# Optimization experiments

Hardware: AMD Instinct MI355X
Metric: run time of the kernel (lower is better)

## Reference

```python
import jax, jax.numpy as jnp
import numpy as np

C_STD = 64                 # len(standard_1020)
CH_NUMS = (1, 4, 16, 64)   # multi-scale channel counts (ms_ch_lst / ch_nums)
BETA = 0.25
DECAY = 0.99
RESI = 0.5                 # abs(quant_resi) for shared Phi


def l2norm(t, eps=1e-12):
    return t / jnp.maximum(jnp.linalg.norm(t, axis=-1, keepdims=True), eps)


def phi_apply(h_LND, w, b):
    # Phi: y = (1-r)*h + r*Conv1d(h), conv over the channel-position axis, feature dim D
    x = jnp.swapaxes(h_LND, 1, 2)                      # (L, D, Nch)
    y = jax.lax.conv_general_dilated(x, w, (1,), 'SAME',
                                     dimension_numbers=('NCH', 'OIH', 'NCH'))
    y = y + b[None, :, None]
    y = jnp.swapaxes(y, 1, 2)                          # (L, Nch, D)
    return h_LND * (1.0 - RESI) + y * RESI


def setup_inputs() -> dict:
    key = jax.random.key(0)
    ks = jax.random.split(key, 5)
    B, T, D, V = 64, 16, 256, 8192
    N = T * C_STD
    z = jax.random.normal(ks[0], (B, N, D), jnp.float32)
    # per-sample permutation of the 64 standard channel ids in the first C_STD slots
    perm = jnp.argsort(jax.random.uniform(ks[1], (B, C_STD)), axis=1).astype(jnp.int32)
    input_chans = jnp.concatenate([perm, jnp.zeros((B, N - C_STD), jnp.int32)], axis=1)
    # tokens ordered time-major: token j has time index j // C_STD
    input_time = jnp.broadcast_to((jnp.arange(N) // C_STD)[None, :], (B, N)).astype(jnp.int32)
    embedding = jax.random.normal(ks[2], (V, D), jnp.float32) * (D ** -0.5 / 36.0)
    phi_w = jax.random.normal(ks[3], (D, D, 3), jnp.float32) * (1.0 / np.sqrt(3.0 * D))
    phi_b = jnp.zeros((D,), jnp.float32)
    cluster_size = jnp.zeros((V,), jnp.float32)
    return {"z": z, "input_chans": input_chans, "input_time": input_time,
            "embedding": embedding, "phi_w": phi_w, "phi_b": phi_b,
            "cluster_size": cluster_size}


def reference(z, input_chans, input_time, embedding, phi_w, phi_b, cluster_size):
    B, N, D = z.shape
    T = N // C_STD
    V = embedding.shape[0]
    z = l2norm(z)
    chans = input_chans[:, :C_STD]                     # (B, 64) channel ids
    # ch_trans: scatter tokens into standard channel layout -> (L, C_STD, D), L = B*T
    z_btcd = z.reshape(B, T, C_STD, D)
    z_LND = jax.vmap(lambda zb, cb: jnp.zeros((T, C_STD, D), z.dtype).at[:, cb].set(zb))(z_btcd, chans)
    z_LND = z_LND.reshape(B * T, C_STD, D)
    L = B * T

    f_no_grad = jax.lax.stop_gradient(z_LND)
    f_rest = f_no_grad
    f_hat = jnp.zeros_like(f_rest)
    e_n = l2norm(embedding)                            # normalized codebook (V, D)

    SN = len(CH_NUMS)
    loss = jnp.zeros((), z.dtype)
    counts = jnp.zeros((V,), z.dtype)
    idx_list = []
    for g in CH_NUMS:                                  # multi-scale residual VQ over channels
        rest_g = f_rest.reshape(L, g, C_STD // g, D).mean(axis=2)   # group_chans_by_mean
        q = l2norm(rest_g)
        logits = jnp.einsum('lgd,vd->lgv', q, e_n)     # cosine sim == -0.5*l2 dist + const
        idx = jnp.argmax(logits, axis=-1)              # (L, g)
        idx_list.append(idx)
        h_g = e_n[idx]                                 # codebook lookup (L, g, D)
        h = jnp.repeat(h_g, C_STD // g, axis=1)        # expand_chans_by_copy -> (L, 64, D)
        h = phi_apply(h, phi_w, phi_b)                 # shared Phi residual conv
        f_hat = f_hat + h
        f_rest = f_rest - h
        loss = loss + BETA * jnp.mean((jax.lax.stop_gradient(f_hat) - z_LND) ** 2) \
                    + jnp.mean((f_hat - f_no_grad) ** 2)
        counts = counts.at[idx.reshape(-1)].add(1.0)   # EMA cluster-size scatter
    loss = loss / SN

    # straight-through: value = f_hat, gradient flows to z
    f_hat_st = jax.lax.stop_gradient(f_hat) + (z_LND - f_no_grad)
    # ch_intrans: gather back to original per-sample channel ordering
    zq_btcd = jax.vmap(lambda fb, cb: fb[:, cb])(f_hat_st.reshape(B, T, C_STD, D), chans)
    z_q = zq_btcd.reshape(B, N, D)

    cluster_size_new = DECAY * cluster_size + (1.0 - DECAY) * counts
    idx_all = jnp.concatenate(idx_list, axis=1)        # (L, sum(CH_NUMS))
    return z_q, loss, idx_all, cluster_size_new
```

## Files before the change

### kernel.cpp

```cpp
#include <hip/hip_runtime.h>

#define D_DIM 256
#define V_DIM 8192
#define L_DIM 1024
#define NROW 65536
#define NELEM 16777216

#define OUT_LOSS 16777216
#define OUT_IDX  16777217
#define OUT_CS   16864257

#define EN_OFF    ((size_t)0)
#define ENH_OFF   ((size_t)2097152)
#define ESUM_OFF  ((size_t)3145728)
#define E0_OFF    ((size_t)5242880)
#define E2_OFF    ((size_t)7340032)
#define WSUM_OFF  ((size_t)9437184)
#define W0_OFF    ((size_t)9502720)
#define W2_OFF    ((size_t)9568256)
#define FREST_OFF ((size_t)9633792)
#define QF_OFF    ((size_t)26411008)
#define QH_OFF    ((size_t)43188224)
#define PTOP_OFF  ((size_t)51576832)
#define IDXI_OFF  ((size_t)52625408)
#define CNT_OFF   ((size_t)52712448)
#define LOSSP_OFF ((size_t)52720640)
#define RNORM_OFF ((size_t)52722688)
#define INV_OFF   ((size_t)52788224)

typedef __attribute__((ext_vector_type(8))) short bf16x8;
typedef __attribute__((ext_vector_type(4))) float f32x4;

__device__ __forceinline__ unsigned int umaxu(unsigned int a, unsigned int b) { return a > b ? a : b; }
__device__ __forceinline__ unsigned int uminu(unsigned int a, unsigned int b) { return a < b ? a : b; }

__device__ __forceinline__ unsigned short f2b(float x) {
    unsigned int u = __float_as_uint(x);
    unsigned int r = (u + 0x7FFFu + ((u >> 16) & 1u)) >> 16;
    return (unsigned short)r;
}

__device__ __forceinline__ void gl_lds16(const void* g, void* l) {
    __builtin_amdgcn_global_load_lds(
        (const __attribute__((address_space(1))) unsigned int*)g,
        (__attribute__((address_space(3))) unsigned int*)l, 16, 0, 0);
}

__device__ __forceinline__ float blk_reduce_sum(float v, float* sb) {
#pragma unroll
    for (int off = 32; off; off >>= 1) v += __shfl_down(v, off, 64);
    const int w = threadIdx.x >> 6;
    if ((threadIdx.x & 63) == 0) sb[w] = v;
    __syncthreads();
    return sb[0] + sb[1] + sb[2] + sb[3];
}

__global__ void k_norm_embed(const float* __restrict__ emb, float* __restrict__ en,
                             unsigned short* __restrict__ enh) {
    __shared__ float sb[4];
    const int v = blockIdx.x, o = threadIdx.x;
    const float x = emb[(size_t)v * 256 + o];
    const float ss = blk_reduce_sum(x * x, sb);
    const float sc = 1.0f / fmaxf(sqrtf(ss), 1e-12f);
    const float y = x * sc;
    en[(size_t)v * 256 + o] = y;
    enh[(size_t)v * 256 + o] = f2b(y);
}

__global__ void k_prep_w(const float* __restrict__ pw, float* __restrict__ wsum,
                         float* __restrict__ w0, float* __restrict__ w2) {
    const int i = blockIdx.x * 256 + threadIdx.x;
    const float a = pw[(size_t)i * 3 + 0];
    const float b = pw[(size_t)i * 3 + 1];
    const float c = pw[(size_t)i * 3 + 2];
    wsum[i] = a + b + c; w0[i] = a; w2[i] = c;
}

__global__ __launch_bounds__(256) void k_phi_gemm(
    const float* __restrict__ en, const float* __restrict__ wsum,
    const float* __restrict__ w0, const float* __restrict__ w2,
    float* __restrict__ esum, float* __restrict__ e0, float* __restrict__ e2) {
    __shared__ __align__(16) float smem[4096];
    float (*As)[128] = (float (*)[128])smem;
    float (*Bs)[128] = (float (*)[128])(smem + 2048);
    const float* Bm; float* Cm;
    if (blockIdx.z == 0)      { Bm = wsum; Cm = esum; }
    else if (blockIdx.z == 1) { Bm = w0;   Cm = e0;   }
    else                      { Bm = w2;   Cm = e2;   }
    const int tid = threadIdx.x, tx = tid & 15, ty = tid >> 4;
    const int rowbase = blockIdx.x * 128, colbase = blockIdx.y * 128;
    float acc[8][8];
#pragma unroll
    for (int r = 0; r < 8; r++)
#pragma unroll
        for (int c = 0; c < 8; c++) acc[r][c] = 0.f;
    for (int kb = 0; kb < 256; kb += 16) {
        __syncthreads();
        {
            const int lr = tid >> 1, k0 = (tid & 1) << 3;
            const float4* ap = (const float4*)(en + ((size_t)(rowbase + lr)) * 256 + kb + k0);
            const float4 a0 = ap[0], a1 = ap[1];
            const float4* bp = (const float4*)(Bm + ((size_t)(colbase + lr)) * 256 + kb + k0);
            const float4 b0 = bp[0], b1 = bp[1];
            As[k0+0][lr]=a0.x; As[k0+1][lr]=a0.y; As[k0+2][lr]=a0.z; As[k0+3][lr]=a0.w;
            As[k0+4][lr]=a1.x; As[k0+5][lr]=a1.y; As[k0+6][lr]=a1.z; As[k0+7][lr]=a1.w;
            Bs[k0+0][lr]=b0.x; Bs[k0+1][lr]=b0.y; Bs[k0+2][lr]=b0.z; Bs[k0+3][lr]=b0.w;
            Bs[k0+4][lr]=b1.x; Bs[k0+5][lr]=b1.y; Bs[k0+6][lr]=b1.z; Bs[k0+7][lr]=b1.w;
        }
        __syncthreads();
#pragma unroll
        for (int k = 0; k < 16; k++) {
            const float4 av0 = *(const float4*)&As[k][ty << 3];
            const float4 av1 = *(const float4*)&As[k][(ty << 3) + 4];
            const float4 bv0 = *(const float4*)&Bs[k][tx << 3];
            const float4 bv1 = *(const float4*)&Bs[k][(tx << 3) + 4];
            const float a[8] = {av0.x, av0.y, av0.z, av0.w, av1.x, av1.y, av1.z, av1.w};
            const float b[8] = {bv0.x, bv0.y, bv0.z, bv0.w, bv1.x, bv1.y, bv1.z, bv1.w};
#pragma unroll
            for (int r = 0; r < 8; r++)
#pragma unroll
                for (int c = 0; c < 8; c++) acc[r][c] = fmaf(a[r], b[c], acc[r][c]);
        }
    }
#pragma unroll
    for (int r = 0; r < 8; r++) {
        float4 o0 = {acc[r][0], acc[r][1], acc[r][2], acc[r][3]};
        float4 o1 = {acc[r][4], acc[r][5], acc[r][6], acc[r][7]};
        float* cp = Cm + ((size_t)(rowbase + (ty << 3) + r)) * 256 + colbase + (tx << 3);
        *(float4*)cp = o0; *(float4*)(cp + 4) = o1;
    }
}

__global__ void k_invperm(const int* __restrict__ ichans, int* __restrict__ inv) {
    const int b = blockIdx.x, c = threadIdx.x;
    inv[(b << 6) + ichans[(b << 10) + c]] = c;
}

__global__ void k_scatter(const float* __restrict__ z, const int* __restrict__ ichans,
                          float* __restrict__ frest, float* __restrict__ rnorm) {
    __shared__ float sb[4];
    const int zrow = blockIdx.x;
    const int b = zrow >> 10, n = zrow & 1023;
    const int t = n >> 6, c = n & 63;
    const int o = threadIdx.x;
    const float x = z[(size_t)zrow * 256 + o];
    const float ss = blk_reduce_sum(x * x, sb);
    const float sc = 1.0f / fmaxf(sqrtf(ss), 1e-12f);
    const int ch = ichans[(b << 10) + c];
    frest[((size_t)(((b << 4) + t) * 64 + ch)) * 256 + o] = x * sc;
    if (o == 0) rnorm[zrow] = sc;
}

__global__ void k_groupq(const float* __restrict__ frest, float* __restrict__ qf,
                         unsigned short* __restrict__ qh, int g, int s) {
    __shared__ float sb[4];
    const int r = blockIdx.x;
    const int l = r / g, j = r - l * g;
    const int o = threadIdx.x;
    const float* base = frest + ((size_t)l * 64 + (size_t)j * s) * 256 + o;
    float acc = 0.f;
    for (int cc = 0; cc < s; cc++) acc += base[(size_t)cc * 256];
    acc *= (1.0f / (float)s);
    const float ss = blk_reduce_sum(acc * acc, sb);
    const float sc = 1.0f / fmaxf(sqrtf(ss), 1e-12f);
    const float qv = acc * sc;
    qf[(size_t)r * 256 + o] = qv;
    qh[(size_t)r * 256 + o] = f2b(qv);
}

__global__ __launch_bounds__(256, 3) void k_amax1(
    const unsigned short* __restrict__ qh, const unsigned short* __restrict__ enh,
    uint2* __restrict__ ptop, int NC, int colsPerChunk) {
    __shared__ unsigned short As[4096];
    __shared__ unsigned short Bs[4096];
    const int tid = threadIdx.x;
    const int lane = tid & 63;
    const int m = lane & 15, q4 = lane >> 4;
    const int w = tid >> 6;
    const int wr = w >> 1, wc = w & 1;
    const int rowbase = blockIdx.x * 128;
    const int chunk = blockIdx.y;
    const int srow = tid >> 2, sgr = tid & 3;

    const unsigned short* qa0 = qh + (size_t)(rowbase + srow) * 256 + sgr * 8;
    const unsigned short* qa1 = qa0 + 64 * 256;
    unsigned short* lA0 = &As[tid * 8];
    unsigned short* lA1 = &As[2048 + tid * 8];
    unsigned short* lB0 = &Bs[tid * 8];
    unsigned short* lB1 = &Bs[2048 + tid * 8];

    unsigned int t1[4][4], t2[4][4];
#pragma unroll
    for (int i = 0; i < 4; i++)
#pragma unroll
        for (int r = 0; r < 4; r++) { t1[i][r] = 0u; t2[i][r] = 0u; }

    const int ntiles = colsPerChunk >> 7;
    for (int nt = 0; nt < ntiles; nt++) {
        const int colchunk = chunk * colsPerChunk + nt * 128;
        const unsigned short* ba0 = enh + (size_t)(colchunk + srow) * 256 + sgr * 8;
        const unsigned short* ba1 = ba0 + 64 * 256;
        f32x4 acc[4][4];
#pragma unroll
        for (int i = 0; i < 4; i++)
#pragma unroll
            for (int j = 0; j < 4; j++) acc[i][j] = (f32x4){0.f, 0.f, 0.f, 0.f};

        for (int kb = 0; kb < 256; kb += 32) {
            __syncthreads();
            gl_lds16(qa0 + kb, lA0);
            gl_lds16(qa1 + kb, lA1);
            gl_lds16(ba0 + kb, lB0);
            gl_lds16(ba1 + kb, lB1);
            __syncthreads();
            bf16x8 af[4], bfr[4];
#pragma unroll
            for (int i = 0; i < 4; i++)
                af[i] = *(const bf16x8*)&As[(wr * 64 + i * 16 + m) * 32 + q4 * 8];
#pragma unroll
            for (int j = 0; j < 4; j++)
                bfr[j] = *(const bf16x8*)&Bs[(wc * 64 + j * 16 + m) * 32 + q4 * 8];
#pragma unroll
            for (int i = 0; i < 4; i++)
#pragma unroll
                for (int j = 0; j < 4; j++)
                    acc[i][j] = __builtin_amdgcn_mfma_f32_16x16x32_bf16(af[i], bfr[j], acc[i][j], 0, 0, 0);
        }
#pragma unroll
        for (int j = 0; j < 4; j++) {
            const unsigned int ct = 8191u - (unsigned int)(colchunk + wc * 64 + j * 16 + m);
#pragma unroll
            for (int i = 0; i < 4; i++)
#pragma unroll
                for (int r = 0; r < 4; r++) {
                    const float wv = acc[i][j][r] + 1.25f;
                    const unsigned int cand = (__float_as_uint(wv) & 0xFFFFE000u) | ct;
                    const unsigned int nb1 = umaxu(t1[i][r], cand);
                    t2[i][r] = umaxu(t2[i][r], uminu(t1[i][r], cand));
                    t1[i][r] = nb1;
                }
        }
    }
    unsigned int mb1[4][4], mb2[4][4];
#pragma unroll
    for (int i = 0; i < 4; i++)
#pragma unroll
        for (int r = 0; r < 4; r++) {
            unsigned int b1 = t1[i][r], b2 = t2[i][r];
#pragma unroll
            for (int d = 1; d < 16; d <<= 1) {
                const unsigned int o1 = (unsigned int)__shfl_xor((int)b1, d, 64);
                const unsigned int o2 = (unsigned int)__shfl_xor((int)b2, d, 64);
                const unsigned int mn = uminu(b1, o1);
                b1 = umaxu(b1, o1);
                b2 = umaxu(mn, umaxu(b2, o2));
            }
            mb1[i][r] = b1; mb2[i][r] = b2;
        }
    __syncthreads();
    uint2* msh = (uint2*)As;
    if (wc == 1 && m == 0) {
#pragma unroll
        for (int i = 0; i < 4; i++)
#pragma unroll
            for (int r = 0; r < 4; r++)
                msh[wr * 64 + i * 16 + q4 * 4 + r] = make_uint2(mb1[i][r], mb2[i][r]);
    }
    __syncthreads();
    if (wc == 0 && m == 0) {
#pragma unroll
        for (int i = 0; i < 4; i++)
#pragma unroll
            for (int r = 0; r < 4; r++) {
                const int rl = wr * 64 + i * 16 + q4 * 4 + r;
                const uint2 o = msh[rl];
                unsigned int b1 = mb1[i][r], b2 = mb2[i][r];
                const unsigned int mn = uminu(b1, o.x);
                b1 = umaxu(b1, o.x);
                b2 = umaxu(mn, umaxu(b2, o.y));
                ptop[(size_t)(rowbase + rl) * NC + chunk] = make_uint2(b1, b2);
            }
    }
}

__global__ __launch_bounds__(256) void k_amax2(
    const uint2* __restrict__ ptop, const float* __restrict__ qf,
    const float* __restrict__ en, int* __restrict__ idxout,
    float* __restrict__ counts, int R, int NC) {
    __shared__ uint2 stop;
    __shared__ double swv[4];
    __shared__ int swi[4];
    const int r = blockIdx.x;
    const int tid = threadIdx.x, lane = tid & 63, w = tid >> 6;
    const uint2* pp = ptop + (size_t)r * NC;
    if (w == 0) {
        const uint2 p = (lane < NC) ? pp[lane] : make_uint2(0u, 0u);
        unsigned int b1 = p.x, b2 = p.y;
#pragma unroll
        for (int d = 1; d < 64; d <<= 1) {
            const unsigned int o1 = (unsigned int)__shfl_xor((int)b1, d, 64);
            const unsigned int o2 = (unsigned int)__shfl_xor((int)b2, d, 64);
            const unsigned int mn = uminu(b1, o1);
            b1 = umaxu(b1, o1);
            b2 = umaxu(mn, umaxu(b2, o2));
        }
        if (lane == 0) stop = make_uint2(b1, b2);
    }
    __syncthreads();
    const unsigned int b1 = stop.x, b2 = stop.y;
    const float* qp = qf + (size_t)r * 256;
    const float4 aq = *(const float4*)(qp + lane * 4);
    const bool ambig = (b1 & 0xFFFFE000u) - (b2 & 0xFFFFE000u) < 32768u;
    if (ambig) {
        double bv = -1e300; int bi = 0x7fffffff;
        const int ncand = 2 * NC;
        for (int ci = w; ci < ncand; ci += 4) {
            const uint2 p = pp[ci >> 1];
            const int col = 8191 - (int)(((ci & 1) ? p.y : p.x) & 0x1FFFu);
            const float4 be = *(const float4*)(en + (size_t)col * 256 + lane * 4);
            double s = (double)aq.x * be.x + (double)aq.y * be.y +
                       (double)aq.z * be.z + (double)aq.w * be.w;
#pragma unroll
            for (int d = 1; d < 64; d <<= 1) s += __shfl_xor(s, d, 64);
            if (s > bv || (s == bv && col < bi)) { bv = s; bi = col; }
        }
        if (lane == 0) { swv[w] = bv; swi[w] = bi; }
        __syncthreads();
        if (tid == 0) {
            double bvv = swv[0]; int bii = swi[0];
            for (int i = 1; i < 4; i++)
                if (swv[i] > bvv || (swv[i] == bvv && swi[i] < bii)) { bvv = swv[i]; bii = swi[i]; }
            idxout[r] = bii;
            atomicAdd(&counts[bii], 1.0f);
        }
    } else if (w == 0) {
        const int c1 = 8191 - (int)(b1 & 0x1FFFu);
        const int c2 = 8191 - (int)(b2 & 0x1FFFu);
        const float4 e1 = *(const float4*)(en + (size_t)c1 * 256 + lane * 4);
        const float4 e2v = *(const float4*)(en + (size_t)c2 * 256 + lane * 4);
        double s1 = (double)aq.x * e1.x + (double)aq.y * e1.y +
                    (double)aq.z * e1.z + (double)aq.w * e1.w;
        double s2 = (double)aq.x * e2v.x + (double)aq.y * e2v.y +
                    (double)aq.z * e2v.z + (double)aq.w * e2v.w;
#pragma unroll
        for (int d = 1; d < 64; d <<= 1) { s1 += __shfl_xor(s1, d, 64); s2 += __shfl_xor(s2, d, 64); }
        if (lane == 0) {
            const int best = (s2 > s1 || (s2 == s1 && c2 < c1)) ? c2 : c1;
            idxout[r] = best;
            atomicAdd(&counts[best], 1.0f);
        }
    }
}

__global__ void k_epilogue(float* __restrict__ frest, const float* __restrict__ en,
    const float* __restrict__ esum, const float* __restrict__ e0, const float* __restrict__ e2,
    const float* __restrict__ bias, const int* __restrict__ idx,
    int g, int slog, int smask, double* __restrict__ lossp,
    int emitQ, float* __restrict__ qf, unsigned short* __restrict__ qh,
    int emitOut, const float* __restrict__ z, const float* __restrict__ rnorm,
    const int* __restrict__ inv, float* __restrict__ out) {
    __shared__ float sb[4];
    const int row = blockIdx.x;
    const int l = row >> 6, ch = row & 63;
    const int j = ch >> slog;
    const int r = l * g + j;
    const int i0 = idx[r];
    const int o = threadIdx.x;
    const size_t b0 = (size_t)i0 * 256 + o;
    float v = 0.5f * en[b0] + 0.5f * (esum[b0] + bias[o]);
    const int chs = ch & smask;
    if (chs == 0) {
        float t = -e0[b0];
        if (j > 0) t += e0[(size_t)idx[r - 1] * 256 + o];
        v += 0.5f * t;
    }
    if (chs == smask) {
        float t = -e2[b0];
        if (j < g - 1) t += e2[(size_t)idx[r + 1] * 256 + o];
        v += 0.5f * t;
    }
    const float nv = frest[(size_t)row * 256 + o] - v;
    const float ss = blk_reduce_sum(nv * nv, sb);
    if (o == 0) atomicAdd(&lossp[blockIdx.x & 255], (double)ss);
    if (emitOut) {
        const int b = l >> 4, t_ = l & 15;
        const int c = inv[(b << 6) + ch];
        const size_t zr = (size_t)((b << 10) + (t_ << 6) + c);
        out[zr * 256 + o] = z[zr * 256 + o] * rnorm[zr] - nv;
    } else {
        frest[(size_t)row * 256 + o] = nv;
        if (emitQ) {
            const float sc = 1.0f / fmaxf(sqrtf(ss), 1e-12f);
            const float qv = nv * sc;
            qf[(size_t)row * 256 + o] = qv;
            qh[(size_t)row * 256 + o] = f2b(qv);
        }
    }
}

__global__ void k_losssum(const double* __restrict__ lossp, float* __restrict__ out) {
    __shared__ double sb[4];
    double s = 0.0;
    for (int i = threadIdx.x; i < 1024; i += 256) s += lossp[i];
#pragma unroll
    for (int off = 32; off; off >>= 1) s += __shfl_down(s, off, 64);
    if ((threadIdx.x & 63) == 0) sb[threadIdx.x >> 6] = s;
    __syncthreads();
    if (threadIdx.x == 0)
        out[OUT_LOSS] = (float)((sb[0] + sb[1] + sb[2] + sb[3]) * (1.25 / 4.0) / 16777216.0);
}

__global__ void k_final(const int* __restrict__ idxi, const float* __restrict__ counts,
                        const float* __restrict__ csin, float* __restrict__ out) {
    const int i = blockIdx.x * 256 + threadIdx.x;
    if (i < 87040) {
        const int l = i / 85, t = i - l * 85;
        int v;
        if (t == 0)       v = idxi[l];
        else if (t < 5)   v = idxi[1024 + l * 4 + (t - 1)];
        else if (t < 21)  v = idxi[5120 + l * 16 + (t - 5)];
        else              v = idxi[21504 + l * 64 + (t - 21)];
        out[OUT_IDX + i] = (float)v;
    } else if (i < 87040 + 8192) {
        const int v = i - 87040;
        out[OUT_CS + v] = 0.99f * csin[v] + 0.01f * counts[v];
    }
}

extern "C" void kernel_launch(void* const* d_in, const int* in_sizes, int n_in,
                              void* d_out, int out_size, void* d_ws, size_t ws_size,
                              hipStream_t stream) {
    (void)in_sizes; (void)n_in; (void)out_size; (void)ws_size;
    const float* z      = (const float*)d_in[0];
    const int*   ichans = (const int*)d_in[1];
    const float* emb    = (const float*)d_in[3];
    const float* phiw   = (const float*)d_in[4];
    const float* phib   = (const float*)d_in[5];
    const float* csin   = (const float*)d_in[6];
    float* ws  = (float*)d_ws;
    float* out = (float*)d_out;

    float* en    = ws + EN_OFF;
    unsigned short* enh = (unsigned short*)(ws + ENH_OFF);
    float* esum  = ws + ESUM_OFF;
    float* e0    = ws + E0_OFF;
    float* e2    = ws + E2_OFF;
    float* wsum  = ws + WSUM_OFF;
    float* w0    = ws + W0_OFF;
    float* w2    = ws + W2_OFF;
    float* frest = ws + FREST_OFF;
    float* qf    = ws + QF_OFF;
    unsigned short* qh = (unsigned short*)(ws + QH_OFF);
    uint2* ptop  = (uint2*)(ws + PTOP_OFF);
    int*   idxi  = (int*)(ws + IDXI_OFF);
    float* counts = ws + CNT_OFF;
    double* lossp = (double*)(ws + LOSSP_OFF);
    float* rnorm = ws + RNORM_OFF;
    int*   inv   = (int*)(ws + INV_OFF);

    hipMemsetAsync(counts, 0, 8192 * sizeof(float) + 1024 * sizeof(double), stream);

    k_norm_embed<<<V_DIM, 256, 0, stream>>>(emb, en, enh);
    k_prep_w<<<256, 256, 0, stream>>>(phiw, wsum, w0, w2);
    k_phi_gemm<<<dim3(V_DIM / 128, 2, 3), 256, 0, stream>>>(en, wsum, w0, w2, esum, e0, e2);
    k_invperm<<<64, 64, 0, stream>>>(ichans, inv);
    k_scatter<<<NROW, 256, 0, stream>>>(z, ichans, frest, rnorm);

    const int gs[4]    = {1, 4, 16, 64};
    const int ncs[4]   = {64, 32, 16, 8};
    const int cpcs[4]  = {128, 256, 512, 1024};
    const int offs[4]  = {0, 1024, 5120, 21504};
    const int slogs[4] = {6, 4, 2, 0};
    for (int st = 0; st < 4; st++) {
        const int g = gs[st], s = 64 / g, NC = ncs[st], R = L_DIM * g;
        if (st < 3)
            k_groupq<<<R, 256, 0, stream>>>(frest, qf, qh, g, s);
        k_amax1<<<dim3(R / 128, NC), 256, 0, stream>>>(qh, enh, ptop, NC, cpcs[st]);
        k_amax2<<<R, 256, 0, stream>>>(ptop, qf, en, idxi + offs[st], counts, R, NC);
        k_epilogue<<<NROW, 256, 0, stream>>>(frest, en, esum, e0, e2, phib, idxi + offs[st],
                                             g, slogs[st], s - 1, lossp + st * 256,
                                             (st == 2) ? 1 : 0, qf, qh,
                                             (st == 3) ? 1 : 0, z, rnorm, inv, out);
    }

    k_losssum<<<1, 256, 0, stream>>>(lossp, out);
    k_final<<<372, 256, 0, stream>>>(idxi, counts, csin, out);
}
```

Before: 1.359 ms.

## Double-buffer argmax GEMM tiles and fuse group quantization into epilogue

The argmax GEMM kernel now double-buffers its LDS tiles across a flattened tile/k loop, so the next slice is fetched while the MFMAs run, which removes one barrier per step. The 1.25 offset is folded into the accumulator initial value. The epilogue now processes several rows per block, matching the next stage's group size, and computes the group mean and normalized query itself. This removes the separate k_groupq launches for stages 1-3 and the extra pass over frest. For stage 3 (rpb=1) the Q emission simply reproduces the old per-row normalization. Fewer epilogue blocks in early stages may reduce parallelism, and the group mean is accumulated in a different order than before.

```diff
diff --git a/kernel.cpp b/kernel.cpp
--- a/kernel.cpp
+++ b/kernel.cpp
@@ -171,8 +171,8 @@
 __global__ __launch_bounds__(256, 3) void k_amax1(
     const unsigned short* __restrict__ qh, const unsigned short* __restrict__ enh,
     uint2* __restrict__ ptop, int NC, int colsPerChunk) {
-    __shared__ unsigned short As[4096];
-    __shared__ unsigned short Bs[4096];
+    __shared__ unsigned short As[2][4096];
+    __shared__ unsigned short Bs[2][4096];
     const int tid = threadIdx.x;
     const int lane = tid & 63;
     const int m = lane & 15, q4 = lane >> 4;
@@ -180,65 +180,74 @@
     const int wr = w >> 1, wc = w & 1;
     const int rowbase = blockIdx.x * 128;
     const int chunk = blockIdx.y;
+    const int colbase0 = chunk * colsPerChunk;
     const int srow = tid >> 2, sgr = tid & 3;
 
     const unsigned short* qa0 = qh + (size_t)(rowbase + srow) * 256 + sgr * 8;
     const unsigned short* qa1 = qa0 + 64 * 256;
-    unsigned short* lA0 = &As[tid * 8];
-    unsigned short* lA1 = &As[2048 + tid * 8];
-    unsigned short* lB0 = &Bs[tid * 8];
-    unsigned short* lB1 = &Bs[2048 + tid * 8];
+    const unsigned short* eb0 = enh + (size_t)srow * 256 + sgr * 8;
+    const unsigned short* eb1 = eb0 + 64 * 256;
+    const int loff = tid * 8;
 
     unsigned int t1[4][4], t2[4][4];
+    f32x4 acc[4][4];
 #pragma unroll
     for (int i = 0; i < 4; i++)
 #pragma unroll
-        for (int r = 0; r < 4; r++) { t1[i][r] = 0u; t2[i][r] = 0u; }
-
-    const int ntiles = colsPerChunk >> 7;
-    for (int nt = 0; nt < ntiles; nt++) {
-        const int colchunk = chunk * colsPerChunk + nt * 128;
-        const unsigned short* ba0 = enh + (size_t)(colchunk + srow) * 256 + sgr * 8;
-        const unsigned short* ba1 = ba0 + 64 * 256;
-        f32x4 acc[4][4];
+        for (int r = 0; r < 4; r++) {
+            t1[i][r] = 0u; t2[i][r] = 0u;
+            acc[i][r] = (f32x4){1.25f, 1.25f, 1.25f, 1.25f};
+        }
+
+    const int nsteps = (colsPerChunk >> 7) * 8;
+    {
+        gl_lds16(qa0, &As[0][loff]);
+        gl_lds16(qa1, &As[0][2048 + loff]);
+        const size_t bgo = (size_t)colbase0 * 256;
+        gl_lds16(eb0 + bgo, &Bs[0][loff]);
+        gl_lds16(eb1 + bgo, &Bs[0][2048 + loff]);
+    }
+    for (int step = 0; step < nsteps; step++) {
+        const int buf = step & 1;
+        __syncthreads();
+        if (step + 1 < nsteps) {
+            const int kb1 = (step + 1) & 7;
+            const int tile1 = (step + 1) >> 3;
+            gl_lds16(qa0 + kb1 * 32, &As[buf ^ 1][loff]);
+            gl_lds16(qa1 + kb1 * 32, &As[buf ^ 1][2048 + loff]);
+            const size_t bgo = (size_t)(colbase0 + tile1 * 128) * 256 + kb1 * 32;
+            gl_lds16(eb0 + bgo, &Bs[buf ^ 1][loff]);
+            gl_lds16(eb1 + bgo, &Bs[buf ^ 1][2048 + loff]);
+        }
+        bf16x8 af[4], bfr[4];
 #pragma unroll
         for (int i = 0; i < 4; i++)
-#pragma unroll
-            for (int j = 0; j < 4; j++) acc[i][j] = (f32x4){0.f, 0.f, 0.f, 0.f};
-
-        for (int kb = 0; kb < 256; kb += 32) {
-            __syncthreads();
-            gl_lds16(qa0 + kb, lA0);
-            gl_lds16(qa1 + kb, lA1);
-            gl_lds16(ba0 + kb, lB0);
-            gl_lds16(ba1 + kb, lB1);
-            __syncthreads();
-            bf16x8 af[4], bfr[4];
-#pragma unroll
-            for (int i = 0; i < 4; i++)
-                af[i] = *(const bf16x8*)&As[(wr * 64 + i * 16 + m) * 32 + q4 * 8];
+            af[i] = *(const bf16x8*)&As[buf][(wr * 64 + i * 16 + m) * 32 + q4 * 8];
+#pragma unroll
+        for (int j = 0; j < 4; j++)
+            bfr[j] = *(const bf16x8*)&Bs[buf][(wc * 64 + j * 16 + m) * 32 + q4 * 8];
+#pragma unroll
+        for (int i = 0; i < 4; i++)
 #pragma unroll
             for (int j = 0; j < 4; j++)
-                bfr[j] = *(const bf16x8*)&Bs[(wc * 64 + j * 16 + m) * 32 + q4 * 8];
-#pragma unroll
-            for (int i = 0; i < 4; i++)
-#pragma unroll
-                for (int j = 0; j < 4; j++)
-                    acc[i][j] = __builtin_amdgcn_mfma_f32_16x16x32_bf16(af[i], bfr[j], acc[i][j], 0, 0, 0);
-        }
-#pragma unroll
-        for (int j = 0; j < 4; j++) {
-            const unsigned int ct = 8191u - (unsigned int)(colchunk + wc * 64 + j * 16 + m);
-#pragma unroll
-            for (int i = 0; i < 4; i++)
-#pragma unroll
-                for (int r = 0; r < 4; r++) {
-                    const float wv = acc[i][j][r] + 1.25f;
-                    const unsigned int cand = (__float_as_uint(wv) & 0xFFFFE000u) | ct;
-                    const unsigned int nb1 = umaxu(t1[i][r], cand);
-                    t2[i][r] = umaxu(t2[i][r], uminu(t1[i][r], cand));
-                    t1[i][r] = nb1;
-                }
+                acc[i][j] = __builtin_amdgcn_mfma_f32_16x16x32_bf16(af[i], bfr[j], acc[i][j], 0, 0, 0);
+        if ((step & 7) == 7) {
+            const int colchunk = colbase0 + (step >> 3) * 128;
+#pragma unroll
+            for (int j = 0; j < 4; j++) {
+                const unsigned int ct = 8191u - (unsigned int)(colchunk + wc * 64 + j * 16 + m);
+#pragma unroll
+                for (int i = 0; i < 4; i++)
+#pragma unroll
+                    for (int r = 0; r < 4; r++) {
+                        const unsigned int cand =
+                            (__float_as_uint(acc[i][j][r]) & 0xFFFFE000u) | (ct & 0x1FFFu);
+                        const unsigned int nb1 = umaxu(t1[i][r], cand);
+                        t2[i][r] = umaxu(t2[i][r], uminu(t1[i][r], cand));
+                        t1[i][r] = nb1;
+                        acc[i][j][r] = 1.25f;
+                    }
+            }
         }
     }
     unsigned int mb1[4][4], mb2[4][4];
@@ -258,7 +267,7 @@
             mb1[i][r] = b1; mb2[i][r] = b2;
         }
     __syncthreads();
-    uint2* msh = (uint2*)As;
+    uint2* msh = (uint2*)&As[0][0];
     if (wc == 1 && m == 0) {
 #pragma unroll
         for (int i = 0; i < 4; i++)
@@ -352,49 +361,68 @@
     }
 }
 
-__global__ void k_epilogue(float* __restrict__ frest, const float* __restrict__ en,
+__global__ __launch_bounds__(256) void k_epi(
+    float* __restrict__ frest, const float* __restrict__ en,
     const float* __restrict__ esum, const float* __restrict__ e0, const float* __restrict__ e2,
     const float* __restrict__ bias, const int* __restrict__ idx,
-    int g, int slog, int smask, double* __restrict__ lossp,
+    int g, int slog, int smask, double* __restrict__ lossp, int rpb,
     int emitQ, float* __restrict__ qf, unsigned short* __restrict__ qh,
     int emitOut, const float* __restrict__ z, const float* __restrict__ rnorm,
     const int* __restrict__ inv, float* __restrict__ out) {
-    __shared__ float sb[4];
-    const int row = blockIdx.x;
-    const int l = row >> 6, ch = row & 63;
-    const int j = ch >> slog;
-    const int r = l * g + j;
-    const int i0 = idx[r];
+    __shared__ float sb[8];
+    const int bid = blockIdx.x;
     const int o = threadIdx.x;
-    const size_t b0 = (size_t)i0 * 256 + o;
-    float v = 0.5f * en[b0] + 0.5f * (esum[b0] + bias[o]);
-    const int chs = ch & smask;
-    if (chs == 0) {
-        float t = -e0[b0];
-        if (j > 0) t += e0[(size_t)idx[r - 1] * 256 + o];
-        v += 0.5f * t;
-    }
-    if (chs == smask) {
-        float t = -e2[b0];
-        if (j < g - 1) t += e2[(size_t)idx[r + 1] * 256 + o];
-        v += 0.5f * t;
-    }
-    const float nv = frest[(size_t)row * 256 + o] - v;
-    const float ss = blk_reduce_sum(nv * nv, sb);
-    if (o == 0) atomicAdd(&lossp[blockIdx.x & 255], (double)ss);
-    if (emitOut) {
-        const int b = l >> 4, t_ = l & 15;
-        const int c = inv[(b << 6) + ch];
-        const size_t zr = (size_t)((b << 10) + (t_ << 6) + c);
-        out[zr * 256 + o] = z[zr * 256 + o] * rnorm[zr] - nv;
-    } else {
-        frest[(size_t)row * 256 + o] = nv;
-        if (emitQ) {
-            const float sc = 1.0f / fmaxf(sqrtf(ss), 1e-12f);
-            const float qv = nv * sc;
-            qf[(size_t)row * 256 + o] = qv;
-            qh[(size_t)row * 256 + o] = f2b(qv);
-        }
+    const int row0 = bid * rpb;
+    const int l = row0 >> 6;
+    float qacc = 0.f, lsum = 0.f;
+    for (int rr = 0; rr < rpb; rr++) {
+        const int row = row0 + rr;
+        const int ch = row & 63;
+        const int j = ch >> slog;
+        const int r = l * g + j;
+        const int i0 = idx[r];
+        const size_t b0 = (size_t)i0 * 256 + o;
+        float v = 0.5f * en[b0] + 0.5f * (esum[b0] + bias[o]);
+        const int chs = ch & smask;
+        if (chs == 0) {
+            float t = -e0[b0];
+            if (j > 0) t += e0[(size_t)idx[r - 1] * 256 + o];
+            v += 0.5f * t;
+        }
+        if (chs == smask) {
+            float t = -e2[b0];
+            if (j < g - 1) t += e2[(size_t)idx[r + 1] * 256 + o];
+            v += 0.5f * t;
+        }
+        const float nv = frest[(size_t)row * 256 + o] - v;
+        qacc += nv; lsum = fmaf(nv, nv, lsum);
+        if (emitOut) {
+            const int b = l >> 4, t_ = l & 15;
+            const int c = inv[(b << 6) + ch];
+            const size_t zr = (size_t)((b << 10) + (t_ << 6) + c);
+            out[zr * 256 + o] = z[zr * 256 + o] * rnorm[zr] - nv;
+        } else {
+            frest[(size_t)row * 256 + o] = nv;
+        }
+    }
+    const float qm = qacc * (1.0f / (float)rpb);
+    float a = lsum, bq = qm * qm;
+#pragma unroll
+    for (int off = 32; off; off >>= 1) {
+        a += __shfl_down(a, off, 64);
+        bq += __shfl_down(bq, off, 64);
+    }
+    const int w = o >> 6;
+    if ((o & 63) == 0) { sb[w] = a; sb[4 + w] = bq; }
+    __syncthreads();
+    if (o == 0)
+        atomicAdd(&lossp[bid & 255], (double)(sb[0] + sb[1] + sb[2] + sb[3]));
+    if (emitQ) {
+        const float qs = sb[4] + sb[5] + sb[6] + sb[7];
+        const float sc = 1.0f / fmaxf(sqrtf(qs), 1e-12f);
+        const float qv = qm * sc;
+        qf[(size_t)bid * 256 + o] = qv;
+        qh[(size_t)bid * 256 + o] = f2b(qv);
     }
 }
 
@@ -465,22 +493,23 @@
     k_phi_gemm<<<dim3(V_DIM / 128, 2, 3), 256, 0, stream>>>(en, wsum, w0, w2, esum, e0, e2);
     k_invperm<<<64, 64, 0, stream>>>(ichans, inv);
     k_scatter<<<NROW, 256, 0, stream>>>(z, ichans, frest, rnorm);
+    k_groupq<<<L_DIM, 256, 0, stream>>>(frest, qf, qh, 1, 64);
 
     const int gs[4]    = {1, 4, 16, 64};
     const int ncs[4]   = {64, 32, 16, 8};
     const int cpcs[4]  = {128, 256, 512, 1024};
     const int offs[4]  = {0, 1024, 5120, 21504};
     const int slogs[4] = {6, 4, 2, 0};
+    const int rpbs[4]  = {16, 4, 1, 1};
     for (int st = 0; st < 4; st++) {
         const int g = gs[st], s = 64 / g, NC = ncs[st], R = L_DIM * g;
-        if (st < 3)
-            k_groupq<<<R, 256, 0, stream>>>(frest, qf, qh, g, s);
         k_amax1<<<dim3(R / 128, NC), 256, 0, stream>>>(qh, enh, ptop, NC, cpcs[st]);
         k_amax2<<<R, 256, 0, stream>>>(ptop, qf, en, idxi + offs[st], counts, R, NC);
-        k_epilogue<<<NROW, 256, 0, stream>>>(frest, en, esum, e0, e2, phib, idxi + offs[st],
-                                             g, slogs[st], s - 1, lossp + st * 256,
-                                             (st == 2) ? 1 : 0, qf, qh,
-                                             (st == 3) ? 1 : 0, z, rnorm, inv, out);
+        k_epi<<<NROW / rpbs[st], 256, 0, stream>>>(frest, en, esum, e0, e2, phib,
+                                                   idxi + offs[st], g, slogs[st], s - 1,
+                                                   lossp + st * 256, rpbs[st],
+                                                   (st < 3) ? 1 : 0, qf, qh,
+                                                   (st == 3) ? 1 : 0, z, rnorm, inv, out);
     }
 
     k_losssum<<<1, 256, 0, stream>>>(lossp, out);
```

Result: faster. 1.184 ms (-12.8%).
